# Performance work log

Measured on AMD Instinct MI355X. Metric: run time of the kernel, lower is better.

The kernel has to match this reference:

```python
import jax, jax.numpy as jnp
import numpy as np

D_MODEL = 512
NUM_HEADS = 8
HEAD_DIM = D_MODEL // NUM_HEADS  # 64


def setup_inputs() -> dict:
    key = jax.random.key(0)
    k_x, k_wqkv, k_bqkv, k_wout, k_bout = jax.random.split(key, 5)
    B, L = 30, 2048
    s_in = 1.0 / np.sqrt(D_MODEL)
    return {
        "x": jax.random.normal(k_x, (B, L, D_MODEL), dtype=jnp.float32),
        "w_qkv": jax.random.uniform(k_wqkv, (3 * D_MODEL, D_MODEL), minval=-s_in, maxval=s_in, dtype=jnp.float32),
        "b_qkv": jax.random.uniform(k_bqkv, (3 * D_MODEL,), minval=-s_in, maxval=s_in, dtype=jnp.float32),
        "w_out": jax.random.uniform(k_wout, (D_MODEL, D_MODEL), minval=-s_in, maxval=s_in, dtype=jnp.float32),
        "b_out": jax.random.uniform(k_bout, (D_MODEL,), minval=-s_in, maxval=s_in, dtype=jnp.float32),
    }


def reference(x, w_qkv, b_qkv, w_out, b_out):
    B, L, _ = x.shape
    # QKV projection: (B, L, 3*d_model)
    qkv = jnp.einsum("bld,ed->ble", x, w_qkv) + b_qkv
    # NOTE: source discards the permute, so layout stays (B, L, H, 3*head_dim)
    qkv = qkv.reshape(B, L, NUM_HEADS, 3 * HEAD_DIM)
    q, k, v = jnp.split(qkv, 3, axis=-1)  # each (B, L, H, head_dim)
    # Attention contracts head_dim -> (B, L, H, H): attention OVER HEADS, faithful to bug
    scores = jnp.einsum("blhd,blgd->blhg", q, k) / np.sqrt(HEAD_DIM)
    # mask=False in source adds 0 -> no-op
    attn = jax.nn.softmax(scores, axis=-1)
    val = jnp.einsum("blhg,blgd->blhd", attn, v).reshape(B, L, D_MODEL)
    out = jnp.einsum("bld,ed->ble", val, w_out) + b_out
    return out
```

## Files before the change

### kernel.cpp

```cpp
#include <hip/hip_runtime.h>
#include <hip/hip_bf16.h>
#include <stdint.h>

typedef short    s16x8  __attribute__((ext_vector_type(8)));
typedef __bf16   bf16x8 __attribute__((ext_vector_type(8)));
typedef float    f32x4  __attribute__((ext_vector_type(4)));

__device__ __forceinline__ unsigned short f2bf(float f) {
    union { float f; unsigned u; } v; v.f = f;
    unsigned r = v.u + 0x7FFFu + ((v.u >> 16) & 1u);
    return (unsigned short)(r >> 16);
}
__device__ __forceinline__ float bf2f(unsigned short s) {
    union { unsigned u; float f; } v; v.u = ((unsigned)s) << 16;
    return v.f;
}

__device__ __forceinline__ void gload16(const void* g, void* l) {
    __builtin_amdgcn_global_load_lds(
        (const __attribute__((address_space(1))) void*)(uintptr_t)g,
        (__attribute__((address_space(3))) void*)(uintptr_t)l,
        16, 0, 0);
}

__global__ __launch_bounds__(256) void cvt_bf16(const float* __restrict__ in,
                                                unsigned short* __restrict__ out,
                                                int n4) {
    int i = blockIdx.x * blockDim.x + threadIdx.x;
    int stride = gridDim.x * blockDim.x;
    for (; i < n4; i += stride) {
        const float4 v = *(const float4*)(in + (size_t)i * 4);
        ushort4 o;
        o.x = f2bf(v.x); o.y = f2bf(v.y); o.z = f2bf(v.z); o.w = f2bf(v.w);
        *(ushort4*)(out + (size_t)i * 4) = o;
    }
}

template<int K, bool OUT_BF16>
__global__ __launch_bounds__(512, 2) void gemm256(
        const unsigned short* __restrict__ A,
        const unsigned short* __restrict__ B,
        const float* __restrict__ bias,
        void* __restrict__ Cvoid,
        int M, int N, int ntn) {
    constexpr int BM = 256, BN = 256, BK = 32, NT = K / BK;
    __shared__ unsigned short As[4][BM * BK];
    __shared__ unsigned short Bs[4][BN * BK];
    const int tid  = threadIdx.x;
    const int lane = tid & 63;
    const int wv   = tid >> 6;
    const int nwg = (int)gridDim.x;
    const int wg  = ((int)blockIdx.x & 7) * (nwg >> 3) + ((int)blockIdx.x >> 3);
    const int bm  = wg / ntn;
    const int bn  = wg % ntn;
    const int wr  = (wv >> 2) * 128;
    const int wc  = (wv & 3) * 64;
    const int lr  = lane & 15;
    const int ls  = lane >> 4;

    const unsigned short* Ag = A + (size_t)bm * BM * K;
    const unsigned short* Bg = B + (size_t)bn * BN * K;

    auto stage = [&](int t) {
        const unsigned short* GA = Ag + t * BK;
        const unsigned short* GB = Bg + t * BK;
        char* la = (char*)As[t & 3];
        char* lb = (char*)Bs[t & 3];
        #pragma unroll
        for (int p = 0; p < 2; ++p) {
            const int c     = p * 512 + tid;
            const int row   = c >> 2;
            const int slot  = c & 3;
            const int gslot = slot ^ ((row >> 1) & 3);
            gload16(GA + (size_t)row * K + gslot * 8, la + c * 16);
            gload16(GB + (size_t)row * K + gslot * 8, lb + c * 16);
        }
    };
    auto frag = [&](const unsigned short* lds, int row) -> bf16x8 {
        const int slot = ls ^ ((row >> 1) & 3);
        return *(const bf16x8*)((const char*)lds + row * (BK * 2) + slot * 16);
    };

    f32x4 acc[8][4] = {};

    stage(0); stage(1); stage(2);

    #pragma unroll
    for (int t = 0; t < NT; ++t) {
        if (t <= NT - 3)      asm volatile("s_waitcnt vmcnt(8)" ::: "memory");
        else if (t == NT - 2) asm volatile("s_waitcnt vmcnt(4)" ::: "memory");
        else                  asm volatile("s_waitcnt vmcnt(0)" ::: "memory");
        __builtin_amdgcn_s_barrier();
        if (t + 3 < NT) stage(t + 3);

        const unsigned short* la = As[t & 3];
        const unsigned short* lb = Bs[t & 3];
        bf16x8 af[8], bfr[4];
        #pragma unroll
        for (int m = 0; m < 8; ++m) af[m] = frag(la, wr + m * 16 + lr);
        #pragma unroll
        for (int n = 0; n < 4; ++n) bfr[n] = frag(lb, wc + n * 16 + lr);

        __builtin_amdgcn_s_setprio(1);
        #pragma unroll
        for (int m = 0; m < 8; ++m)
            #pragma unroll
            for (int n = 0; n < 4; ++n)
                acc[m][n] = __builtin_amdgcn_mfma_f32_16x16x32_bf16(
                    af[m], bfr[n], acc[m][n], 0, 0, 0);
        __builtin_amdgcn_s_setprio(0);
    }

    const int r0 = bm * BM + wr + ls * 4;
    const int c0 = bn * BN + wc + lr;
    #pragma unroll
    for (int n = 0; n < 4; ++n) {
        const int gc = c0 + n * 16;
        const float bv = bias[gc];
        #pragma unroll
        for (int m = 0; m < 8; ++m) {
            #pragma unroll
            for (int j = 0; j < 4; ++j) {
                const int gr = r0 + m * 16 + j;
                const float v = acc[m][n][j] + bv;
                if constexpr (OUT_BF16)
                    ((unsigned short*)Cvoid)[(size_t)gr * N + gc] = f2bf(v);
                else
                    ((float*)Cvoid)[(size_t)gr * N + gc] = v;
            }
        }
    }
}

__global__ __launch_bounds__(256) void attn_heads(
        const unsigned short* __restrict__ qkv,
        unsigned short* __restrict__ val,
        int M) {
    const int t    = blockIdx.x * 4 + (threadIdx.x >> 6);
    const int lane = threadIdx.x & 63;
    const int h    = lane >> 3;
    const int c    = lane & 7;
    const unsigned short* base = qkv + (size_t)t * 1536;

    s16x8 q8 = *(const s16x8*)(base + h * 192 + c * 8);
    float qf[8];
    #pragma unroll
    for (int j = 0; j < 8; ++j) qf[j] = bf2f((unsigned short)q8[j]);

    float s[8];
    #pragma unroll
    for (int g = 0; g < 8; ++g) {
        s16x8 k8 = *(const s16x8*)(base + g * 192 + 64 + c * 8);
        float p = 0.f;
        #pragma unroll
        for (int j = 0; j < 8; ++j) p += qf[j] * bf2f((unsigned short)k8[j]);
        s[g] = p;
    }
    #pragma unroll
    for (int mask = 1; mask <= 4; mask <<= 1)
        #pragma unroll
        for (int g = 0; g < 8; ++g)
            s[g] += __shfl_xor(s[g], mask, 64);

    float mx = -1e30f;
    #pragma unroll
    for (int g = 0; g < 8; ++g) { s[g] *= 0.125f; mx = fmaxf(mx, s[g]); }
    float sum = 0.f;
    #pragma unroll
    for (int g = 0; g < 8; ++g) { s[g] = __expf(s[g] - mx); sum += s[g]; }
    const float inv = 1.f / sum;

    float acc[8] = {0.f,0.f,0.f,0.f,0.f,0.f,0.f,0.f};
    #pragma unroll
    for (int g = 0; g < 8; ++g) {
        s16x8 v8 = *(const s16x8*)(base + g * 192 + 128 + c * 8);
        const float ag = s[g] * inv;
        #pragma unroll
        for (int j = 0; j < 8; ++j) acc[j] += ag * bf2f((unsigned short)v8[j]);
    }
    s16x8 ov;
    #pragma unroll
    for (int j = 0; j < 8; ++j) ov[j] = (short)f2bf(acc[j]);
    *(s16x8*)(val + (size_t)t * 512 + h * 64 + c * 8) = ov;
}

extern "C" void kernel_launch(void* const* d_in, const int* in_sizes, int n_in,
                              void* d_out, int out_size, void* d_ws, size_t ws_size,
                              hipStream_t stream) {
    const float* x     = (const float*)d_in[0];
    const float* w_qkv = (const float*)d_in[1];
    const float* b_qkv = (const float*)d_in[2];
    const float* w_out = (const float*)d_in[3];
    const float* b_out = (const float*)d_in[4];
    float* out = (float*)d_out;

    const int DM = 512;
    const int M  = in_sizes[0] / DM;

    unsigned short* xb    = (unsigned short*)d_ws;
    unsigned short* wqkvb = xb + (size_t)M * DM;
    unsigned short* woutb = wqkvb + (size_t)3 * DM * DM;
    unsigned short* qkvb  = woutb + (size_t)DM * DM;
    unsigned short* valb  = xb;

    cvt_bf16<<<2048, 256, 0, stream>>>(x, xb, M * DM / 4);
    cvt_bf16<<<96,   256, 0, stream>>>(w_qkv, wqkvb, 3 * DM * DM / 4);
    cvt_bf16<<<32,   256, 0, stream>>>(w_out, woutb, DM * DM / 4);

    gemm256<512, true><<<dim3((M / 256) * (3 * DM / 256)), 512, 0, stream>>>(
        xb, wqkvb, b_qkv, qkvb, M, 3 * DM, 3 * DM / 256);

    attn_heads<<<M / 4, 256, 0, stream>>>(qkvb, valb, M);

    gemm256<512, false><<<dim3((M / 256) * (DM / 256)), 512, 0, stream>>>(
        valb, woutb, b_out, out, M, DM, DM / 256);
}
```

Measured before the change: 314.5 us.

## Split GEMM k-step into two half-phases interleaving LDS reads, loads and MFMAs

Restructures the gemm256 main loop so each k-step runs as two halves. Each half issues part of the next global-to-LDS prefetch and reads half the A fragments, while MFMAs on the other half run. B fragments and the first A half for the next step are prefetched into double-buffered registers, so LDS reads overlap matrix math instead of waiting before it. This adds extra barriers per iteration, raises register pressure, and makes the vmcnt accounting more intricate.

```diff
diff --git a/kernel.cpp b/kernel.cpp
--- a/kernel.cpp
+++ b/kernel.cpp
@@ -61,20 +61,17 @@
     const unsigned short* Ag = A + (size_t)bm * BM * K;
     const unsigned short* Bg = B + (size_t)bn * BN * K;
 
-    auto stage = [&](int t) {
+    auto stage_half = [&](int t, int h) {
         const unsigned short* GA = Ag + t * BK;
         const unsigned short* GB = Bg + t * BK;
         char* la = (char*)As[t & 3];
         char* lb = (char*)Bs[t & 3];
-        #pragma unroll
-        for (int p = 0; p < 2; ++p) {
-            const int c     = p * 512 + tid;
-            const int row   = c >> 2;
-            const int slot  = c & 3;
-            const int gslot = slot ^ ((row >> 1) & 3);
-            gload16(GA + (size_t)row * K + gslot * 8, la + c * 16);
-            gload16(GB + (size_t)row * K + gslot * 8, lb + c * 16);
-        }
+        const int c     = h * 512 + tid;
+        const int row   = c >> 2;
+        const int slot  = c & 3;
+        const int gslot = slot ^ ((row >> 1) & 3);
+        gload16(GA + (size_t)row * K + gslot * 8, la + c * 16);
+        gload16(GB + (size_t)row * K + gslot * 8, lb + c * 16);
     };
     auto frag = [&](const unsigned short* lds, int row) -> bf16x8 {
         const int slot = ls ^ ((row >> 1) & 3);
@@ -82,33 +79,57 @@
     };
 
     f32x4 acc[8][4] = {};
-
-    stage(0); stage(1); stage(2);
+    bf16x8 bfr[2][4];
+    bf16x8 af0[4], af1[4];
+
+    stage_half(0, 0); stage_half(0, 1);
+    stage_half(1, 0); stage_half(1, 1);
+    stage_half(2, 0); stage_half(2, 1);
+    asm volatile("s_waitcnt vmcnt(8)" ::: "memory");
+    __builtin_amdgcn_s_barrier();
+    #pragma unroll
+    for (int n = 0; n < 4; ++n) bfr[0][n] = frag(Bs[0], wc + n * 16 + lr);
+    #pragma unroll
+    for (int m = 0; m < 4; ++m) af0[m] = frag(As[0], wr + m * 16 + lr);
 
     #pragma unroll
     for (int t = 0; t < NT; ++t) {
-        if (t <= NT - 3)      asm volatile("s_waitcnt vmcnt(8)" ::: "memory");
-        else if (t == NT - 2) asm volatile("s_waitcnt vmcnt(4)" ::: "memory");
-        else                  asm volatile("s_waitcnt vmcnt(0)" ::: "memory");
-        __builtin_amdgcn_s_barrier();
-        if (t + 3 < NT) stage(t + 3);
-
-        const unsigned short* la = As[t & 3];
-        const unsigned short* lb = Bs[t & 3];
-        bf16x8 af[8], bfr[4];
-        #pragma unroll
-        for (int m = 0; m < 8; ++m) af[m] = frag(la, wr + m * 16 + lr);
-        #pragma unroll
-        for (int n = 0; n < 4; ++n) bfr[n] = frag(lb, wc + n * 16 + lr);
-
+        const int cur = t & 1, nxt = cur ^ 1;
+        if (t + 3 < NT) stage_half(t + 3, 0);
+        #pragma unroll
+        for (int m = 0; m < 4; ++m) af1[m] = frag(As[t & 3], wr + 64 + m * 16 + lr);
         __builtin_amdgcn_s_setprio(1);
         #pragma unroll
-        for (int m = 0; m < 8; ++m)
+        for (int m = 0; m < 4; ++m)
             #pragma unroll
             for (int n = 0; n < 4; ++n)
                 acc[m][n] = __builtin_amdgcn_mfma_f32_16x16x32_bf16(
-                    af[m], bfr[n], acc[m][n], 0, 0, 0);
+                    af0[m], bfr[cur][n], acc[m][n], 0, 0, 0);
         __builtin_amdgcn_s_setprio(0);
+        __builtin_amdgcn_s_barrier();
+
+        if (t + 3 < NT) stage_half(t + 3, 1);
+        if (t + 1 < NT) {
+            if (t <= NT - 4)      asm volatile("s_waitcnt vmcnt(8)" ::: "memory");
+            else if (t == NT - 3) asm volatile("s_waitcnt vmcnt(4)" ::: "memory");
+            else                  asm volatile("s_waitcnt vmcnt(0)" ::: "memory");
+            __builtin_amdgcn_s_barrier();
+            #pragma unroll
+            for (int n = 0; n < 4; ++n)
+                bfr[nxt][n] = frag(Bs[(t + 1) & 3], wc + n * 16 + lr);
+            #pragma unroll
+            for (int m = 0; m < 4; ++m)
+                af0[m] = frag(As[(t + 1) & 3], wr + m * 16 + lr);
+        }
+        __builtin_amdgcn_s_setprio(1);
+        #pragma unroll
+        for (int m = 0; m < 4; ++m)
+            #pragma unroll
+            for (int n = 0; n < 4; ++n)
+                acc[4 + m][n] = __builtin_amdgcn_mfma_f32_16x16x32_bf16(
+                    af1[m], bfr[cur][n], acc[4 + m][n], 0, 0, 0);
+        __builtin_amdgcn_s_setprio(0);
+        __builtin_amdgcn_s_barrier();
     }
 
     const int r0 = bm * BM + wr + ls * 4;
```

Result: no change. 314.4 us (-0.0%).

## Restructure GEMM to 4 waves with 128x128 warp tiles and direct A loads

Applied to the files above, without the earlier changes.

The 256x256 GEMM tile now runs on 4 waves instead of 8, and each wave computes a 128x128 sub-tile with 64 accumulators. A fragments are loaded straight from global memory into registers and double-buffered one k-step ahead, so only B is staged through LDS. The aim is to raise MFMA work per LDS read and halve LDS footprint. In exchange, register pressure rises sharply, occupancy is limited to one block, and A reads from global are uncoalesced 16-byte loads per lane.

```diff
diff --git a/kernel.cpp b/kernel.cpp
--- a/kernel.cpp
+++ b/kernel.cpp
@@ -37,84 +37,84 @@
 }
 
 template<int K, bool OUT_BF16>
-__global__ __launch_bounds__(512, 2) void gemm256(
+__global__ __launch_bounds__(256, 1) void gemm4w(
         const unsigned short* __restrict__ A,
         const unsigned short* __restrict__ B,
         const float* __restrict__ bias,
         void* __restrict__ Cvoid,
         int M, int N, int ntn) {
     constexpr int BM = 256, BN = 256, BK = 32, NT = K / BK;
-    __shared__ unsigned short As[4][BM * BK];
     __shared__ unsigned short Bs[4][BN * BK];
     const int tid  = threadIdx.x;
     const int lane = tid & 63;
     const int wv   = tid >> 6;
-    const int nwg = (int)gridDim.x;
-    const int wg  = ((int)blockIdx.x & 7) * (nwg >> 3) + ((int)blockIdx.x >> 3);
-    const int bm  = wg / ntn;
-    const int bn  = wg % ntn;
-    const int wr  = (wv >> 2) * 128;
-    const int wc  = (wv & 3) * 64;
-    const int lr  = lane & 15;
-    const int ls  = lane >> 4;
+    const int nwg  = (int)gridDim.x;
+    const int wg   = ((int)blockIdx.x & 7) * (nwg >> 3) + ((int)blockIdx.x >> 3);
+    const int bm   = wg / ntn;
+    const int bn   = wg % ntn;
+    const int wr   = (wv >> 1) * 128;
+    const int wc   = (wv & 1) * 128;
+    const int lr   = lane & 15;
+    const int ls   = lane >> 4;
 
     const unsigned short* Ag = A + (size_t)bm * BM * K;
     const unsigned short* Bg = B + (size_t)bn * BN * K;
 
-    auto stage = [&](int t) {
-        const unsigned short* GA = Ag + t * BK;
-        const unsigned short* GB = Bg + t * BK;
-        char* la = (char*)As[t & 3];
+    auto stageB = [&](int t) {
         char* lb = (char*)Bs[t & 3];
         #pragma unroll
-        for (int p = 0; p < 2; ++p) {
-            const int c     = p * 512 + tid;
+        for (int p = 0; p < 4; ++p) {
+            const int c     = p * 256 + tid;
             const int row   = c >> 2;
             const int slot  = c & 3;
             const int gslot = slot ^ ((row >> 1) & 3);
-            gload16(GA + (size_t)row * K + gslot * 8, la + c * 16);
-            gload16(GB + (size_t)row * K + gslot * 8, lb + c * 16);
+            gload16(Bg + (size_t)row * K + t * BK + gslot * 8, lb + c * 16);
         }
     };
-    auto frag = [&](const unsigned short* lds, int row) -> bf16x8 {
+    auto fragB = [&](int t, int n) -> bf16x8 {
+        const int row  = wc + n * 16 + lr;
         const int slot = ls ^ ((row >> 1) & 3);
-        return *(const bf16x8*)((const char*)lds + row * (BK * 2) + slot * 16);
+        return *(const bf16x8*)((const char*)Bs[t & 3] + row * (BK * 2) + slot * 16);
     };
-
-    f32x4 acc[8][4] = {};
-
-    stage(0); stage(1); stage(2);
+    auto loadA = [&](int t, bf16x8* dst) {
+        #pragma unroll
+        for (int m = 0; m < 8; ++m)
+            dst[m] = *(const bf16x8*)(Ag + (size_t)(wr + m * 16 + lr) * K
+                                         + t * BK + ls * 8);
+    };
+
+    f32x4 acc[8][8] = {};
+    bf16x8 af[2][8];
+    bf16x8 bf[8];
+
+    stageB(0); stageB(1); stageB(2);
+    loadA(0, af[0]);
 
     #pragma unroll
     for (int t = 0; t < NT; ++t) {
-        if (t <= NT - 3)      asm volatile("s_waitcnt vmcnt(8)" ::: "memory");
-        else if (t == NT - 2) asm volatile("s_waitcnt vmcnt(4)" ::: "memory");
-        else                  asm volatile("s_waitcnt vmcnt(0)" ::: "memory");
+        if (t <= NT - 3)      asm volatile("s_waitcnt vmcnt(16)" ::: "memory");
+        else if (t == NT - 2) asm volatile("s_waitcnt vmcnt(12)" ::: "memory");
+        else                  asm volatile("s_waitcnt vmcnt(8)"  ::: "memory");
         __builtin_amdgcn_s_barrier();
-        if (t + 3 < NT) stage(t + 3);
-
-        const unsigned short* la = As[t & 3];
-        const unsigned short* lb = Bs[t & 3];
-        bf16x8 af[8], bfr[4];
-        #pragma unroll
-        for (int m = 0; m < 8; ++m) af[m] = frag(la, wr + m * 16 + lr);
-        #pragma unroll
-        for (int n = 0; n < 4; ++n) bfr[n] = frag(lb, wc + n * 16 + lr);
+        if (t + 1 < NT) loadA(t + 1, af[(t + 1) & 1]);
+        if (t + 3 < NT) stageB(t + 3);
+        #pragma unroll
+        for (int n = 0; n < 8; ++n) bf[n] = fragB(t, n);
 
         __builtin_amdgcn_s_setprio(1);
         #pragma unroll
-        for (int m = 0; m < 8; ++m)
+        for (int n = 0; n < 8; ++n)
             #pragma unroll
-            for (int n = 0; n < 4; ++n)
+            for (int m = 0; m < 8; ++m)
                 acc[m][n] = __builtin_amdgcn_mfma_f32_16x16x32_bf16(
-                    af[m], bfr[n], acc[m][n], 0, 0, 0);
+                    af[t & 1][m], bf[n], acc[m][n], 0, 0, 0);
         __builtin_amdgcn_s_setprio(0);
     }
 
     const int r0 = bm * BM + wr + ls * 4;
     const int c0 = bn * BN + wc + lr;
     #pragma unroll
-    for (int n = 0; n < 4; ++n) {
+    for (int n = 0; n < 8; ++n) {
         const int gc = c0 + n * 16;
         const float bv = bias[gc];
         #pragma unroll
@@ -207,11 +207,11 @@
     cvt_bf16<<<96,   256, 0, stream>>>(w_qkv, wqkvb, 3 * DM * DM / 4);
     cvt_bf16<<<32,   256, 0, stream>>>(w_out, woutb, DM * DM / 4);
 
-    gemm256<512, true><<<dim3((M / 256) * (3 * DM / 256)), 512, 0, stream>>>(
+    gemm4w<512, true><<<dim3((M / 256) * (3 * DM / 256)), 256, 0, stream>>>(
         xb, wqkvb, b_qkv, qkvb, M, 3 * DM, 3 * DM / 256);
 
     attn_heads<<<M / 4, 256, 0, stream>>>(qkvb, valb, M);
 
-    gemm256<512, false><<<dim3((M / 256) * (DM / 256)), 512, 0, stream>>>(
+    gemm4w<512, false><<<dim3((M / 256) * (DM / 256)), 256, 0, stream>>>(
         valb, woutb, b_out, out, M, DM, DM / 256);
 }
```

Result: slower. 344.9 us (+9.7%).
